# Kernel tuning notes

Hardware: AMD Instinct MI355X
Metric: run time of the kernel (lower is better)

Reference implementation:

```python
import jax, jax.numpy as jnp
import numpy as np

N = 100_000      # nodes
E = 1_600_000    # edges (avg degree 16)
FIN = 128
FOUT = 64
C = 1.0          # Poincare ball curvature (args.c)
T = 0.48         # threshold (forward default)
MIN_NORM = 1e-15
PROJ_EPS = 4e-3  # float32 boundary eps used by standard PoincareBall.proj


def _artanh(x):
    x = jnp.clip(x, -1.0 + 1e-7, 1.0 - 1e-7)
    return 0.5 * (jnp.log1p(x) - jnp.log1p(-x))


def logmap0(p, c):
    sc = c ** 0.5
    n = jnp.clip(jnp.linalg.norm(p, axis=-1, keepdims=True), MIN_NORM, None)
    return p / (sc * n) * _artanh(sc * n)


def expmap0(u, c):
    sc = c ** 0.5
    n = jnp.clip(jnp.linalg.norm(u, axis=-1, keepdims=True), MIN_NORM, None)
    return jnp.tanh(sc * n) * u / (sc * n)


def proj(x, c):
    n = jnp.clip(jnp.linalg.norm(x, axis=-1, keepdims=True), MIN_NORM, None)
    maxn = (1.0 - PROJ_EPS) / (c ** 0.5)
    return jnp.where(n > maxn, x / n * maxn, x)


def setup_inputs() -> dict:
    key = jax.random.key(0)
    k0, k1, k2, k3, k4 = jax.random.split(key, 5)
    # points near the origin of the Poincare ball
    x = jax.random.normal(k0, (N, FIN), dtype=jnp.float32) * 0.05
    edge_index = jax.random.randint(k1, (2, E), 0, N, dtype=jnp.int32)
    W_up = jax.random.normal(k2, (FIN, FOUT), dtype=jnp.float32) / np.float32(np.sqrt(FIN))
    W_pl = jax.random.normal(k3, (FOUT, 2), dtype=jnp.float32) / np.float32(np.sqrt(FOUT))
    W_lw = jax.random.normal(k4, (2 * FOUT, 1), dtype=jnp.float32) / np.float32(np.sqrt(2 * FOUT))
    return {"x": x, "edge_index": edge_index, "W_up": W_up, "W_pl": W_pl, "W_lw": W_lw}


def reference(x, edge_index, W_up, W_pl, W_lw):
    src, dst = edge_index[0], edge_index[1]

    def agg(v):  # PyG add-aggregation: out[i] = sum_{(j->i)} v[j]
        return jax.ops.segment_sum(v[src], dst, num_segments=N)

    x_tan = logmap0(x, C)                                   # [N, FIN]
    updated_x = jax.nn.leaky_relu(x_tan @ W_up)             # [N, FOUT], slope 0.01
    sum_neigh = agg(updated_x)                              # [N, FOUT]
    random_prob = jax.nn.softmax(jax.nn.relu(sum_neigh @ W_pl), axis=-1)  # [N, 2]
    sel_v = jnp.where(random_prob[:, 1:2] > T, 1.0, 0.0)    # [N, 1] hard gate
    sum_sel = agg(sel_v * updated_x)                        # [N, FOUT]
    weight_sel = jax.nn.sigmoid(jnp.concatenate([sum_sel, sum_neigh], axis=-1) @ W_lw)  # [N, 1]
    a_x = jax.nn.relu(agg(weight_sel * sel_v * updated_x))  # [N, FOUT]
    out = updated_x + a_x
    return proj(expmap0(out, C), C)
```

## Files before the change

kernel.cpp:

```cpp
#include <hip/hip_runtime.h>
#include <math.h>

#define FIN 128
#define FOUT 64
#define MAXDEG 64
#define BKT_SHIFT 7
#define BKT_CAP 2560


__device__ __forceinline__ float4 f4add(float4 a, float4 b) {
  return make_float4(a.x + b.x, a.y + b.y, a.z + b.z, a.w + b.w);
}
__device__ __forceinline__ float4 f4fma(float c, float4 v, float4 a) {
  return make_float4(fmaf(c, v.x, a.x), fmaf(c, v.y, a.y),
                     fmaf(c, v.z, a.z), fmaf(c, v.w, a.w));
}
__device__ __forceinline__ float4 f4shflxor(float4 v, int off) {
  return make_float4(__shfl_xor(v.x, off, 64), __shfl_xor(v.y, off, 64),
                     __shfl_xor(v.z, off, 64), __shfl_xor(v.w, off, 64));
}
__device__ __forceinline__ float red16(float v) {
  v += __shfl_xor(v, 1, 64);
  v += __shfl_xor(v, 2, 64);
  v += __shfl_xor(v, 4, 64);
  v += __shfl_xor(v, 8, 64);
  return v;
}
__device__ __forceinline__ float wave_sum(float v) {
#pragma unroll
  for (int off = 1; off <= 32; off <<= 1) v += __shfl_xor(v, off, 64);
  return v;
}

__device__ __forceinline__ float row_scale(float ss) {
  float n  = sqrtf(ss);
  float nc = fmaxf(n, 1e-15f);
  float t  = fminf(nc, 1.0f - 1e-7f);
  float at = 0.5f * (log1pf(t) - log1pf(-t));
  return at / nc;
}

__device__ __forceinline__ float leaky(float v) {
  return (v >= 0.f) ? v : 0.01f * v;
}

__device__ __forceinline__ unsigned int bf16rne(float x) {
  unsigned int b = __float_as_uint(x);
  b += 0x7FFFu + ((b >> 16) & 1u);
  return b >> 16;
}
__device__ __forceinline__ float4 bf4(uint2 v) {
  return make_float4(__uint_as_float(v.x << 16),
                     __uint_as_float(v.x & 0xFFFF0000u),
                     __uint_as_float(v.y << 16),
                     __uint_as_float(v.y & 0xFFFF0000u));
}

__global__ __launch_bounds__(256) void k_main(const float* __restrict__ x,
                                              const float* __restrict__ Wup,
                                              const float* __restrict__ Wpl,
                                              const float* __restrict__ Wlw,
                                              float* __restrict__ u,
                                              float* __restrict__ scl4,
                                              const int* __restrict__ ei, int E,
                                              int nb, int* __restrict__ bcnt,
                                              int2* __restrict__ stg,
                                              int N, int gemmBlocks) {
  __shared__ float buf[2 * 64 * FIN];
  __shared__ float wls[256];
  __shared__ float ps[256];
  __shared__ float scl[128];

  int t = threadIdx.x;

  if (blockIdx.x >= gemmBlocks) {
    int* hist = (int*)buf;
    int* base = hist + nb;
    int bb = blockIdx.x - gemmBlocks;
    for (int h = t; h < nb; h += 256) hist[h] = 0;
    __syncthreads();
    int e0 = bb * 4096 + t * 16;
    int sv[16], dv[16];
#pragma unroll
    for (int j = 0; j < 16; j += 4) {
      int e = e0 + j;
      if (e + 3 < E) {
        int4 s4 = *(const int4*)(ei + e);
        int4 d4 = *(const int4*)(ei + E + e);
        sv[j] = s4.x; sv[j+1] = s4.y; sv[j+2] = s4.z; sv[j+3] = s4.w;
        dv[j] = d4.x; dv[j+1] = d4.y; dv[j+2] = d4.z; dv[j+3] = d4.w;
      } else {
        for (int q = 0; q < 4; ++q) {
          int ee = e + q;
          sv[j+q] = (ee < E) ? ei[ee] : -1;
          dv[j+q] = (ee < E) ? ei[E + ee] : -1;
        }
      }
    }
#pragma unroll
    for (int j = 0; j < 16; ++j)
      if (dv[j] >= 0) atomicAdd(&hist[dv[j] >> BKT_SHIFT], 1);
    __syncthreads();
    for (int h = t; h < nb; h += 256)
      base[h] = hist[h] ? atomicAdd(&bcnt[h], hist[h]) : 0;
    __syncthreads();
    for (int h = t; h < nb; h += 256) hist[h] = 0;
    __syncthreads();
#pragma unroll
    for (int j = 0; j < 16; ++j) {
      if (dv[j] < 0) continue;
      int b = dv[j] >> BKT_SHIFT;
      int p = base[b] + atomicAdd(&hist[b], 1);
      if (p < BKT_CAP) stg[(size_t)b * BKT_CAP + p] = make_int2(sv[j], dv[j]);
    }
    return;
  }

  int n0 = blockIdx.x * 128;
  {
    int proj = t >> 6, f = t & 63;
    float wv = (proj == 0) ? Wpl[f * 2]
             : (proj == 1) ? Wpl[f * 2 + 1]
             : (proj == 2) ? Wlw[f] : Wlw[64 + f];
    wls[t] = wv;
  }
  {
    int n    = t & 127;
    int khal = t >> 7;
    int gn = n0 + n;
    bool ok = gn < N;
    const float4* xr = (const float4*)(x + (size_t)gn * FIN);
    float* xb = buf + (n >> 6) * 8192;
    int nl = n & 63;
#pragma unroll
    for (int m = 0; m < 16; ++m) {
      int kc = khal * 16 + m;
      float4 v = ok ? xr[kc] : make_float4(0.f, 0.f, 0.f, 0.f);
      xb[(kc * 4 + 0) * 64 + nl] = v.x;
      xb[(kc * 4 + 1) * 64 + nl] = v.y;
      xb[(kc * 4 + 2) * 64 + nl] = v.z;
      xb[(kc * 4 + 3) * 64 + nl] = v.w;
    }
  }
  __syncthreads();

  {
    int n = t & 127, part = t >> 7;
    const float* xb = buf + (n >> 6) * 8192;
    int nl = n & 63;
    float s = 0.f;
#pragma unroll
    for (int k = part * 64; k < part * 64 + 64; ++k) {
      float v = xb[k * 64 + nl];
      s = fmaf(v, v, s);
    }
    ps[t] = s;
  }
  __syncthreads();
  if (t < 128) scl[t] = row_scale(ps[t] + ps[t + 128]);
  __syncthreads();

  int wave = t >> 6, lane = t & 63;
  int tile = wave >> 1, half = wave & 1;
  int i = lane & 7, j = lane >> 3;
  const float* xp = buf + tile * 8192 + i * 8;
  const float* wg = Wup + half * 32 + j * 4;
  float4 a0 = make_float4(0,0,0,0), a1 = a0, a2 = a0, a3 = a0;
  float4 a4 = a0, a5 = a0, a6 = a0, a7 = a0;
#pragma unroll 8
  for (int k = 0; k < FIN; ++k) {
    float4 xv0 = *(const float4*)(xp + k * 64);
    float4 xv1 = *(const float4*)(xp + k * 64 + 4);
    float4 wv = *(const float4*)(wg + k * 64);
    a0 = f4fma(xv0.x, wv, a0);
    a1 = f4fma(xv0.y, wv, a1);
    a2 = f4fma(xv0.z, wv, a2);
    a3 = f4fma(xv0.w, wv, a3);
    a4 = f4fma(xv1.x, wv, a4);
    a5 = f4fma(xv1.y, wv, a5);
    a6 = f4fma(xv1.z, wv, a6);
    a7 = f4fma(xv1.w, wv, a7);
  }
  __syncthreads();

  int fbase = half * 32 + j * 4;
#pragma unroll
  for (int r = 0; r < 8; ++r) {
    float4 acc = (r==0)?a0:(r==1)?a1:(r==2)?a2:(r==3)?a3:(r==4)?a4:(r==5)?a5:(r==6)?a6:a7;
    int nn = tile * 64 + i * 8 + r;
    int gn = n0 + nn;
    float sc = scl[nn];
    float4 o = make_float4(leaky(sc * acc.x), leaky(sc * acc.y),
                           leaky(sc * acc.z), leaky(sc * acc.w));
    if (gn < N) *(float4*)(u + (size_t)gn * FOUT + fbase) = o;
    buf[nn * 67 + fbase]     = o.x;
    buf[nn * 67 + fbase + 1] = o.y;
    buf[nn * 67 + fbase + 2] = o.z;
    buf[nn * 67 + fbase + 3] = o.w;
  }
  __syncthreads();

  {
    int proj = t >> 6;
    const float* wc = wls + proj * 64;
#pragma unroll
    for (int rep = 0; rep < 2; ++rep) {
      int n = (t & 63) + rep * 64;
      int gn = n0 + n;
      const float* ur = buf + n * 67;
      float acc = 0.f;
#pragma unroll 8
      for (int f = 0; f < 64; ++f) acc = fmaf(ur[f], wc[f], acc);
      if (gn < N) scl4[(size_t)gn * 4 + proj] = acc;
    }
  }
}

__global__ __launch_bounds__(256) void k_binB(const int2* __restrict__ stg,
                                              const int* __restrict__ bcnt,
                                              int N, int* __restrict__ deg,
                                              int* __restrict__ slots) {
  __shared__ int cur[128];
  int b = blockIdx.x, t = threadIdx.x;
  if (t < 128) cur[t] = 0;
  __syncthreads();
  int cnt = min(bcnt[b], BKT_CAP);
  int dbase = b << BKT_SHIFT;
  const int2* sp = stg + (size_t)b * BKT_CAP;
  for (int i = t; i < cnt; i += 256) {
    int2 e = sp[i];
    int p = atomicAdd(&cur[e.y - dbase], 1);
    if (p < MAXDEG) slots[(size_t)e.y * MAXDEG + p] = e.x;
  }
  __syncthreads();
  if (t < 128) {
    int dst = dbase + t;
    if (dst < N) {
      int c = min(cur[t], MAXDEG);
      deg[dst] = c;
      int cr = (c + 15) & ~15;
      for (int p = c; p < cr; ++p) slots[(size_t)dst * MAXDEG + p] = N;
    }
  }
}

__global__ __launch_bounds__(256) void k_aggA(const int* __restrict__ deg,
                                              const int* __restrict__ slots,
                                              const float4* __restrict__ scl4,
                                              float* __restrict__ selF,
                                              float* __restrict__ gq,
                                              float* __restrict__ tp, int N) {
  int wv = threadIdx.x >> 6, lane = threadIdx.x & 63;
  int i = blockIdx.x * 4 + wv;
  if (i >= N) return;
  int d = deg[i];
  int s = slots[(size_t)i * MAXDEG + lane];
  bool valid = lane < d;
  s = valid ? s : 0;
  float4 g = scl4[s];
  float sp0 = wave_sum(valid ? g.x : 0.f);
  float sp1 = wave_sum(valid ? g.y : 0.f);
  float sq2 = wave_sum(valid ? g.w : 0.f);
  float r0 = fmaxf(sp0, 0.f), r1 = fmaxf(sp1, 0.f);
  float m  = fmaxf(r0, r1);
  float e0 = expf(r0 - m), e1 = expf(r1 - m);
  float p  = e1 / (e0 + e1);
  float sel = (p > 0.48f) ? 1.f : 0.f;
  if (lane == 0) {
    float4 own = scl4[i];
    selF[i] = sel;
    gq[i]   = sel * own.z;
    tp[i]   = sq2;
  }
}

__global__ __launch_bounds__(256) void k_aggB(const int* __restrict__ deg,
                                              const int* __restrict__ slots,
                                              const float* __restrict__ gq,
                                              const float* __restrict__ tp,
                                              const float* __restrict__ selF,
                                              const float* __restrict__ u,
                                              unsigned int* __restrict__ uw,
                                              int N) {
  if (blockIdx.x == 0 && threadIdx.x < 32)
    uw[(size_t)N * 32 + threadIdx.x] = 0u;
  int wv = threadIdx.x >> 6, lane = threadIdx.x & 63;
  int i = blockIdx.x * 4 + wv;
  if (i >= N) return;
  int d = deg[i];
  int s = slots[(size_t)i * MAXDEG + lane];
  bool valid = lane < d;
  s = valid ? s : 0;
  float v = gq[s];
  float t = tp[i] + wave_sum(valid ? v : 0.f);
  float seli = selF[i];
  float val = 0.f;
  if (seli != 0.f) {
    float sig = 1.f / (1.f + expf(-t));
    val = sig * u[(size_t)i * 64 + lane];
  }
  unsigned int b = bf16rne(val);
  unsigned int partner = (unsigned int)__shfl_xor((int)b, 1, 64);
  if ((lane & 1) == 0)
    uw[(size_t)i * 32 + (lane >> 1)] = (b & 0xFFFFu) | (partner << 16);
}

__global__ __launch_bounds__(256) void k_agg3(const int* __restrict__ deg,
                                              const int* __restrict__ slots,
                                              const float* __restrict__ selF,
                                              const float* __restrict__ u,
                                              const uint2* __restrict__ uw,
                                              float* __restrict__ out, int N) {
  __shared__ int comp[4][64];
  int wv = threadIdx.x >> 6, lane = threadIdx.x & 63;
  int i = blockIdx.x * 4 + wv;
  if (i >= N) return;
  int d = deg[i];
  bool valid = lane < d;
  int s = valid ? slots[(size_t)i * MAXDEG + lane] : 0;
  bool flag = valid && (selF[s] != 0.f);
  unsigned long long mask = __ballot(flag);
  int cnt = __popcll(mask);
  comp[wv][lane] = N;
  int rank = __popcll(mask & ((1ull << lane) - 1ull));
  if (flag) comp[wv][rank] = s;
  int sub = lane >> 4, l4 = lane & 15;
  float4 acc0 = make_float4(0, 0, 0, 0), acc1 = acc0;
  for (int k0 = 0; k0 < cnt; k0 += 8) {
    int s0 = comp[wv][k0 + sub];
    int s1 = comp[wv][k0 + sub + 4];
    uint2 w0 = uw[(size_t)s0 * 16 + l4];
    uint2 w1 = uw[(size_t)s1 * 16 + l4];
    acc0 = f4add(acc0, bf4(w0));
    acc1 = f4add(acc1, bf4(w1));
  }
  float4 acc = f4add(acc0, acc1);
  acc = f4add(acc, f4shflxor(acc, 16));
  acc = f4add(acc, f4shflxor(acc, 32));
  float4 uv = ((const float4*)(u + (size_t)i * 64))[l4];
  float4 ov = make_float4(uv.x + fmaxf(acc.x, 0.f), uv.y + fmaxf(acc.y, 0.f),
                          uv.z + fmaxf(acc.z, 0.f), uv.w + fmaxf(acc.w, 0.f));
  float ssp = ov.x * ov.x + ov.y * ov.y + ov.z * ov.z + ov.w * ov.w;
  float ss  = red16(ssp);
  float nc  = fmaxf(sqrtf(ss), 1e-15f);
  float th  = tanhf(nc);
  float fac = th / nc;
  float4 r = make_float4(ov.x * fac, ov.y * fac, ov.z * fac, ov.w * fac);
  float n2 = fmaxf(th, 1e-15f);
  float maxn = 1.0f - 4e-3f;
  float sc = (n2 > maxn) ? (maxn / n2) : 1.0f;
  float4 res = make_float4(r.x * sc, r.y * sc, r.z * sc, r.w * sc);
  if (sub == 0) ((float4*)(out + (size_t)i * 64))[l4] = res;
}

extern "C" void kernel_launch(void* const* d_in, const int* in_sizes, int n_in,
                              void* d_out, int out_size, void* d_ws, size_t ws_size,
                              hipStream_t stream) {
  const float* x   = (const float*)d_in[0];
  const int*   ei  = (const int*)d_in[1];
  const float* Wup = (const float*)d_in[2];
  const float* Wpl = (const float*)d_in[3];
  const float* Wlw = (const float*)d_in[4];
  float* out = (float*)d_out;

  int N = in_sizes[0] / FIN;
  int E = in_sizes[1] / 2;
  int nb = (N + (1 << BKT_SHIFT) - 1) >> BKT_SHIFT;

  char* ws = (char*)d_ws;
  float* u     = (float*)ws;
  int*   slots = (int*)(u + (size_t)N * 64);
  char*  regB  = (char*)(slots + (size_t)N * MAXDEG);
  size_t regB_sz = (size_t)nb * BKT_CAP * sizeof(int2);
  int2*  stg   = (int2*)regB;
  unsigned int* uwp = (unsigned int*)regB;
  float* scl4  = (float*)(regB + regB_sz);
  int*   deg   = (int*)(scl4 + (size_t)N * 4);
  float* selF  = (float*)(deg + N);
  float* gq    = selF + N;
  float* tp    = gq + N;
  int*   bcnt  = (int*)(tp + N);

  hipMemsetAsync(bcnt, 0, nb * sizeof(int), stream);

  int gemmBlocks = (N + 127) / 128;
  int binABlocks = (E + 4095) / 4096;
  k_main<<<gemmBlocks + binABlocks, 256, 0, stream>>>(
      x, Wup, Wpl, Wlw, u, scl4, ei, E, nb, bcnt, stg, N, gemmBlocks);
  k_binB<<<nb, 256, 0, stream>>>(stg, bcnt, N, deg, slots);
  int nblk = (N + 3) / 4;
  k_aggA<<<nblk, 256, 0, stream>>>(deg, slots, (const float4*)scl4, selF, gq, tp, N);
  k_aggB<<<nblk, 256, 0, stream>>>(deg, slots, gq, tp, selF, u, uwp, N);
  k_agg3<<<nblk, 256, 0, stream>>>(deg, slots, selF, u, (const uint2*)uwp, out, N);
}
```

Measured before the change: 244.6 us.

## Split GEMM K-loop in halves, prefetch second half during first, shrink LDS

The fused GEMM block now stages x in two K-halves. The second half is loaded into registers while the first half's FMA loop runs, and the row norm is computed from registers instead of a separate LDS pass. The x buffer drops from 64 KB to about 34 KB of LDS, which can raise occupancy, at the cost of 64 extra live registers for the prefetch. The aggregation kernels also now guard the slots load so lanes past the degree skip the memory read.

```diff
diff --git a/kernel.cpp b/kernel.cpp
--- a/kernel.cpp
+++ b/kernel.cpp
@@ -66,7 +66,7 @@
                                               int nb, int* __restrict__ bcnt,
                                               int2* __restrict__ stg,
                                               int N, int gemmBlocks) {
-  __shared__ float buf[2 * 64 * FIN];
+  __shared__ float buf[128 * 67];
   __shared__ float wls[256];
   __shared__ float ps[256];
   __shared__ float scl[128];
@@ -124,51 +124,49 @@
              : (proj == 2) ? Wlw[f] : Wlw[64 + f];
     wls[t] = wv;
   }
-  {
-    int n    = t & 127;
-    int khal = t >> 7;
-    int gn = n0 + n;
-    bool ok = gn < N;
-    const float4* xr = (const float4*)(x + (size_t)gn * FIN);
-    float* xb = buf + (n >> 6) * 8192;
-    int nl = n & 63;
-#pragma unroll
-    for (int m = 0; m < 16; ++m) {
-      int kc = khal * 16 + m;
-      float4 v = ok ? xr[kc] : make_float4(0.f, 0.f, 0.f, 0.f);
-      xb[(kc * 4 + 0) * 64 + nl] = v.x;
-      xb[(kc * 4 + 1) * 64 + nl] = v.y;
-      xb[(kc * 4 + 2) * 64 + nl] = v.z;
-      xb[(kc * 4 + 3) * 64 + nl] = v.w;
-    }
-  }
-  __syncthreads();
-
-  {
-    int n = t & 127, part = t >> 7;
-    const float* xb = buf + (n >> 6) * 8192;
-    int nl = n & 63;
-    float s = 0.f;
-#pragma unroll
-    for (int k = part * 64; k < part * 64 + 64; ++k) {
-      float v = xb[k * 64 + nl];
-      s = fmaf(v, v, s);
-    }
-    ps[t] = s;
-  }
-  __syncthreads();
-  if (t < 128) scl[t] = row_scale(ps[t] + ps[t + 128]);
-  __syncthreads();
+
+  int n    = t & 127;
+  int khal = t >> 7;
+  int gn = n0 + n;
+  bool ok = gn < N;
+  const float4* xr = (const float4*)(x + (size_t)gn * FIN);
+  float* xb = buf + (n >> 6) * 4096;
+  int nl = n & 63;
 
   int wave = t >> 6, lane = t & 63;
   int tile = wave >> 1, half = wave & 1;
   int i = lane & 7, j = lane >> 3;
-  const float* xp = buf + tile * 8192 + i * 8;
+  const float* xp = buf + tile * 4096 + i * 8;
   const float* wg = Wup + half * 32 + j * 4;
   float4 a0 = make_float4(0,0,0,0), a1 = a0, a2 = a0, a3 = a0;
   float4 a4 = a0, a5 = a0, a6 = a0, a7 = a0;
+  float ssum = 0.f;
+
+  float4 r0[8], r1[8];
+#pragma unroll
+  for (int m = 0; m < 8; ++m) {
+    int kcg = khal * 8 + m;
+    r0[m] = ok ? xr[kcg] : make_float4(0.f, 0.f, 0.f, 0.f);
+  }
+#pragma unroll
+  for (int m = 0; m < 8; ++m) {
+    float4 v = r0[m];
+    ssum = fmaf(v.x, v.x, fmaf(v.y, v.y, fmaf(v.z, v.z, fmaf(v.w, v.w, ssum))));
+    int kl = (khal * 8 + m) * 4;
+    xb[(kl + 0) * 64 + nl] = v.x;
+    xb[(kl + 1) * 64 + nl] = v.y;
+    xb[(kl + 2) * 64 + nl] = v.z;
+    xb[(kl + 3) * 64 + nl] = v.w;
+  }
+#pragma unroll
+  for (int m = 0; m < 8; ++m) {
+    int kcg = 16 + khal * 8 + m;
+    r1[m] = ok ? xr[kcg] : make_float4(0.f, 0.f, 0.f, 0.f);
+  }
+  __syncthreads();
+
 #pragma unroll 8
-  for (int k = 0; k < FIN; ++k) {
+  for (int k = 0; k < 64; ++k) {
     float4 xv0 = *(const float4*)(xp + k * 64);
     float4 xv1 = *(const float4*)(xp + k * 64 + 4);
     float4 wv = *(const float4*)(wg + k * 64);
@@ -183,16 +181,46 @@
   }
   __syncthreads();
 
+#pragma unroll
+  for (int m = 0; m < 8; ++m) {
+    float4 v = r1[m];
+    ssum = fmaf(v.x, v.x, fmaf(v.y, v.y, fmaf(v.z, v.z, fmaf(v.w, v.w, ssum))));
+    int kl = (khal * 8 + m) * 4;
+    xb[(kl + 0) * 64 + nl] = v.x;
+    xb[(kl + 1) * 64 + nl] = v.y;
+    xb[(kl + 2) * 64 + nl] = v.z;
+    xb[(kl + 3) * 64 + nl] = v.w;
+  }
+  ps[t] = ssum;
+  __syncthreads();
+  if (t < 128) scl[t] = row_scale(ps[t] + ps[t + 128]);
+
+#pragma unroll 8
+  for (int k = 0; k < 64; ++k) {
+    float4 xv0 = *(const float4*)(xp + k * 64);
+    float4 xv1 = *(const float4*)(xp + k * 64 + 4);
+    float4 wv = *(const float4*)(wg + (64 + k) * 64);
+    a0 = f4fma(xv0.x, wv, a0);
+    a1 = f4fma(xv0.y, wv, a1);
+    a2 = f4fma(xv0.z, wv, a2);
+    a3 = f4fma(xv0.w, wv, a3);
+    a4 = f4fma(xv1.x, wv, a4);
+    a5 = f4fma(xv1.y, wv, a5);
+    a6 = f4fma(xv1.z, wv, a6);
+    a7 = f4fma(xv1.w, wv, a7);
+  }
+  __syncthreads();
+
   int fbase = half * 32 + j * 4;
 #pragma unroll
   for (int r = 0; r < 8; ++r) {
     float4 acc = (r==0)?a0:(r==1)?a1:(r==2)?a2:(r==3)?a3:(r==4)?a4:(r==5)?a5:(r==6)?a6:a7;
     int nn = tile * 64 + i * 8 + r;
-    int gn = n0 + nn;
+    int gnn = n0 + nn;
     float sc = scl[nn];
     float4 o = make_float4(leaky(sc * acc.x), leaky(sc * acc.y),
                            leaky(sc * acc.z), leaky(sc * acc.w));
-    if (gn < N) *(float4*)(u + (size_t)gn * FOUT + fbase) = o;
+    if (gnn < N) *(float4*)(u + (size_t)gnn * FOUT + fbase) = o;
     buf[nn * 67 + fbase]     = o.x;
     buf[nn * 67 + fbase + 1] = o.y;
     buf[nn * 67 + fbase + 2] = o.z;
@@ -205,13 +233,13 @@
     const float* wc = wls + proj * 64;
 #pragma unroll
     for (int rep = 0; rep < 2; ++rep) {
-      int n = (t & 63) + rep * 64;
-      int gn = n0 + n;
-      const float* ur = buf + n * 67;
+      int nn = (t & 63) + rep * 64;
+      int gnn = n0 + nn;
+      const float* ur = buf + nn * 67;
       float acc = 0.f;
 #pragma unroll 8
       for (int f = 0; f < 64; ++f) acc = fmaf(ur[f], wc[f], acc);
-      if (gn < N) scl4[(size_t)gn * 4 + proj] = acc;
+      if (gnn < N) scl4[(size_t)gnn * 4 + proj] = acc;
     }
   }
 }
@@ -254,9 +282,9 @@
   int i = blockIdx.x * 4 + wv;
   if (i >= N) return;
   int d = deg[i];
-  int s = slots[(size_t)i * MAXDEG + lane];
   bool valid = lane < d;
-  s = valid ? s : 0;
+  int s = 0;
+  if (valid) s = slots[(size_t)i * MAXDEG + lane];
   float4 g = scl4[s];
   float sp0 = wave_sum(valid ? g.x : 0.f);
   float sp1 = wave_sum(valid ? g.y : 0.f);
@@ -288,9 +316,9 @@
   int i = blockIdx.x * 4 + wv;
   if (i >= N) return;
   int d = deg[i];
-  int s = slots[(size_t)i * MAXDEG + lane];
   bool valid = lane < d;
-  s = valid ? s : 0;
+  int s = 0;
+  if (valid) s = slots[(size_t)i * MAXDEG + lane];
   float v = gq[s];
   float t = tp[i] + wave_sum(valid ? v : 0.f);
   float seli = selF[i];
@@ -317,7 +345,8 @@
   if (i >= N) return;
   int d = deg[i];
   bool valid = lane < d;
-  int s = valid ? slots[(size_t)i * MAXDEG + lane] : 0;
+  int s = 0;
+  if (valid) s = slots[(size_t)i * MAXDEG + lane];
   bool flag = valid && (selF[s] != 0.f);
   unsigned long long mask = __ballot(flag);
   int cnt = __popcll(mask);
```

Measured after the change: 292.4 us. 1.2x slower.
